# Optimization experiments

Hardware: AMD Instinct MI355X
Metric: run time of the kernel (lower is better)

The kernel has to match this reference:

```python
import jax, jax.numpy as jnp
import numpy as np

NUM_REL = 3


def _inter_layer(h_tail_all, self_tail, self_full, adj, idx, alpha):
    """One InterAgg layer (vectorized over 3 relations' IntraAgg + softmax fusion).
    h_tail_all: [N, d]  last-d features of previous layer for ALL nodes
    self_tail:  [n, d]  same features for the batch nodes
    self_full:  [n, D]  full previous-layer features for the batch nodes
    adj:        [3, N, K] neighbor indices
    idx:        [n]      batch node indices
    alpha:      [2d, 3]  relation attention params
    returns [n, D + 2d]
    """
    W = jax.nn.softmax(alpha, axis=1)  # [2d, 3]
    weighted = jnp.zeros((idx.shape[0], alpha.shape[0]), dtype=h_tail_all.dtype)
    for r in range(NUM_REL):  # fixed small structural loop
        neigh = adj[r][idx]                       # [n, K]
        mean = h_tail_all[neigh].mean(axis=1)     # [n, d]  neighbor-mean (IntraAgg _feats_1)
        intra = jnp.concatenate([mean, self_tail - mean], axis=1)  # [n, 2d]
        weighted = weighted + intra * W[:, r]     # softmax-weighted relation fusion
    return jnp.concatenate([self_full, weighted], axis=1)


def setup_inputs() -> dict:
    key = jax.random.key(0)
    ks = jax.random.split(key, 8)
    N, K, d, B = 50000, 32, 64, 1024
    return {
        "feat_data": jax.random.normal(ks[0], (N, 25), dtype=jnp.float32),
        "W_mlp": jax.random.normal(ks[1], (25, d), dtype=jnp.float32) * 0.2,
        "alpha1": jax.random.normal(ks[2], (2 * d, 3), dtype=jnp.float32) * 0.1,
        "alpha2": jax.random.normal(ks[3], (4 * d, 3), dtype=jnp.float32) * 0.1,
        "linear_w": jax.random.normal(ks[4], (7 * d, 2), dtype=jnp.float32) * 0.05,
        "prior": jax.random.uniform(ks[5], (2,), dtype=jnp.float32, minval=0.01, maxval=1.0),
        "adj": jax.random.randint(ks[6], (3, N, K), 0, N, dtype=jnp.int32),
        "nodes": jax.random.randint(ks[7], (B,), 0, N, dtype=jnp.int32),
    }


def reference(feat_data, W_mlp, alpha1, alpha2, linear_w, prior, adj, nodes):
    N = feat_data.shape[0]
    d = W_mlp.shape[1]
    # MLP layer (layer 0): per-node linear projection
    h0 = feat_data @ W_mlp                                   # [N, d]
    # InterAgg layer 1 over all nodes (so layer 2 can gather neighbor features)
    all_idx = jnp.arange(N)
    h1 = _inter_layer(h0, h0, h0, adj, all_idx, alpha1)      # [N, 3d]
    # InterAgg layer 2 over the batch nodes; uses last 2d cols of layer-1 output
    self_full = h1[nodes]                                    # [B, 3d]
    self_tail = self_full[:, -2 * d:]                        # [B, 2d]
    h2 = _inter_layer(h1[:, -2 * d:], self_tail, self_full, adj, nodes, alpha2)  # [B, 7d]
    # Final linear + log-prior
    return h2 @ linear_w + jnp.log(prior)                    # [B, 2]
```

## Files before the change

### kernel.cpp

```cpp
#include <hip/hip_runtime.h>

typedef unsigned int u32;
typedef unsigned short u16;

__device__ __forceinline__ float bf16_lo(u32 u) { u32 x = u << 16; return __builtin_bit_cast(float, x); }
__device__ __forceinline__ float bf16_hi(u32 u) { u32 x = u & 0xffff0000u; return __builtin_bit_cast(float, x); }
__device__ __forceinline__ float bf16f(u16 v) { u32 x = ((u32)v) << 16; return __builtin_bit_cast(float, x); }
__device__ __forceinline__ u16 f2bf(float f) {
    u32 x = __builtin_bit_cast(u32, f);
    return (u16)((x + 0x7fffu + ((x >> 16) & 1u)) >> 16);
}

__global__ __launch_bounds__(256) void k_prep(const float* __restrict__ feat,
                                              u16* __restrict__ featp, int N) {
    int t = blockIdx.x * 256 + threadIdx.x;
    int row = t >> 5, col = t & 31;
    if (row >= N) return;
    featp[(size_t)row * 32 + col] = (col < 25) ? f2bf(feat[(size_t)row * 25 + col]) : (u16)0;
}

__global__ __launch_bounds__(256) void k_layer1(const float* __restrict__ feat,
                                                const u16* __restrict__ featp,
                                                const float* __restrict__ Wmlp,
                                                const float* __restrict__ alpha1,
                                                const int* __restrict__ adj,
                                                u16* __restrict__ w1h, int N) {
    int wave = threadIdx.x >> 6;
    int lane = threadIdx.x & 63;
    int i = blockIdx.x * 4 + wave;
    if (i >= N) return;
    int g = lane >> 4;
    int c = lane & 15;

    float wcol[25];
#pragma unroll
    for (int k = 0; k < 25; ++k) wcol[k] = Wmlp[k * 64 + lane];

    const u32* fp = (const u32*)featp;

    float a0[3], a1[3];
#pragma unroll
    for (int r = 0; r < 3; ++r) {
        const int* arow = adj + ((size_t)r * N + i) * 32;
        float s0 = 0.f, s1 = 0.f;
#pragma unroll
        for (int it = 0; it < 8; ++it) {
            int nb = arow[it * 4 + g];
            u32 u = fp[nb * 16 + c];
            s0 += bf16_lo(u);
            s1 += bf16_hi(u);
        }
        s0 += __shfl_xor(s0, 16, 64); s0 += __shfl_xor(s0, 32, 64);
        s1 += __shfl_xor(s1, 16, 64); s1 += __shfl_xor(s1, 32, 64);
        a0[r] = s0; a1[r] = s1;
    }

    float mean[3];
#pragma unroll
    for (int r = 0; r < 3; ++r) {
        float acc = 0.f;
#pragma unroll
        for (int k = 0; k < 25; ++k) {
            int src = (k & 1) ? __builtin_bit_cast(int, a1[r]) : __builtin_bit_cast(int, a0[r]);
            float mf = __builtin_bit_cast(float, __builtin_amdgcn_readlane(src, k >> 1));
            acc += mf * wcol[k];
        }
        mean[r] = acc * (1.f / 32.f);
    }

    const float* frow = feat + (size_t)i * 25;
    float self = 0.f;
#pragma unroll
    for (int k = 0; k < 25; ++k) self += frow[k] * wcol[k];

    float et[3], eb[3], st = 0.f, sb = 0.f;
#pragma unroll
    for (int r = 0; r < 3; ++r) {
        et[r] = __expf(alpha1[lane * 3 + r]);        st += et[r];
        eb[r] = __expf(alpha1[(64 + lane) * 3 + r]); sb += eb[r];
    }
    float top = 0.f, bot = 0.f;
#pragma unroll
    for (int r = 0; r < 3; ++r) { top += et[r] * mean[r]; bot += eb[r] * mean[r]; }
    top /= st;
    bot /= sb;

    w1h[(size_t)i * 128 + lane]      = f2bf(top);
    w1h[(size_t)i * 128 + 64 + lane] = f2bf(self - bot);
}

__global__ __launch_bounds__(128) void k_layer2(const float* __restrict__ feat,
                                                const float* __restrict__ Wmlp,
                                                const u16* __restrict__ w1h,
                                                const float* __restrict__ alpha2,
                                                const float* __restrict__ lw,
                                                const float* __restrict__ prior,
                                                const int* __restrict__ adj,
                                                const int* __restrict__ nodes,
                                                float* __restrict__ out, int N) {
    __shared__ int s_idx[96];
    __shared__ float s_red[4];
    int b = blockIdx.x;
    int i = nodes[b];
    int t = threadIdx.x;

    if (t < 96) {
        int r = t >> 5, k = t & 31;
        s_idx[t] = adj[((size_t)r * N + i) * 32 + k];
    }
    __syncthreads();

    float mean[3];
#pragma unroll
    for (int r = 0; r < 3; ++r) {
        float acc = 0.f;
#pragma unroll
        for (int k = 0; k < 32; ++k)
            acc += bf16f(w1h[(size_t)s_idx[r * 32 + k] * 128 + t]);
        mean[r] = acc * (1.f / 32.f);
    }

    float et[3], eb[3], st = 0.f, sb = 0.f;
#pragma unroll
    for (int r = 0; r < 3; ++r) {
        et[r] = __expf(alpha2[t * 3 + r]);         st += et[r];
        eb[r] = __expf(alpha2[(128 + t) * 3 + r]); sb += eb[r];
    }
    float t2 = 0.f, wb = 0.f;
#pragma unroll
    for (int r = 0; r < 3; ++r) { t2 += et[r] * mean[r]; wb += eb[r] * mean[r]; }
    t2 /= st;
    wb /= sb;

    float t1 = bf16f(w1h[(size_t)i * 128 + t]);
    float t3 = t1 - wb;

    float p0 = t1 * lw[(64 + t) * 2 + 0] + t2 * lw[(192 + t) * 2 + 0] + t3 * lw[(320 + t) * 2 + 0];
    float p1 = t1 * lw[(64 + t) * 2 + 1] + t2 * lw[(192 + t) * 2 + 1] + t3 * lw[(320 + t) * 2 + 1];
    if (t < 64) {
        float t0 = 0.f;
#pragma unroll
        for (int k = 0; k < 25; ++k) t0 += feat[(size_t)i * 25 + k] * Wmlp[k * 64 + t];
        p0 += t0 * lw[t * 2 + 0];
        p1 += t0 * lw[t * 2 + 1];
    }

#pragma unroll
    for (int off = 32; off > 0; off >>= 1) {
        p0 += __shfl_down(p0, off, 64);
        p1 += __shfl_down(p1, off, 64);
    }
    int wv = t >> 6, lane = t & 63;
    if (lane == 0) { s_red[wv * 2 + 0] = p0; s_red[wv * 2 + 1] = p1; }
    __syncthreads();
    if (t == 0) {
        out[b * 2 + 0] = s_red[0] + s_red[2] + __logf(prior[0]);
        out[b * 2 + 1] = s_red[1] + s_red[3] + __logf(prior[1]);
    }
}

extern "C" void kernel_launch(void* const* d_in, const int* in_sizes, int n_in,
                              void* d_out, int out_size, void* d_ws, size_t ws_size,
                              hipStream_t stream) {
    const float* feat   = (const float*)d_in[0];
    const float* Wmlp   = (const float*)d_in[1];
    const float* alpha1 = (const float*)d_in[2];
    const float* alpha2 = (const float*)d_in[3];
    const float* lw     = (const float*)d_in[4];
    const float* prior  = (const float*)d_in[5];
    const int*   adj    = (const int*)d_in[6];
    const int*   nodes  = (const int*)d_in[7];
    float* out = (float*)d_out;

    int N = in_sizes[0] / 25;
    int B = in_sizes[7];

    u16* featp = (u16*)d_ws;
    u16* w1    = featp + (size_t)N * 32;

    k_prep  <<<(N * 32 + 255) / 256, 256, 0, stream>>>(feat, featp, N);
    k_layer1<<<(N + 3) / 4,          256, 0, stream>>>(feat, featp, Wmlp, alpha1, adj, w1, N);
    k_layer2<<<B,                    128, 0, stream>>>(feat, Wmlp, w1, alpha2, lw, prior, adj, nodes, out, N);
}
```

Baseline: 61.69 us.

## Split layer-1 into a gather pass and an MFMA projection with prefolded weights

Layer 1 is split into two kernels. The first gathers the raw neighbor feature sums for each relation, plus each node's own features, into an fp16 staging buffer. The second projects that buffer with a single MFMA matmul against a weight matrix that folds in the MLP weights, the relation softmax, the 1/32 mean and the sign of the difference term. This replaces the per-lane readlane dot products and exp work in layer 1 with matrix-core work. The cost is an extra intermediate buffer written and read back per node, two more kernel launches, and fp16 rounding of the neighbor sums.

New measurement: 66.42 us. +7.7%, slower.

```diff
diff --git a/kernel.cpp b/kernel.cpp
--- a/kernel.cpp
+++ b/kernel.cpp
@@ -2,6 +2,17 @@
 
 typedef unsigned int u32;
 typedef unsigned short u16;
+typedef _Float16 f16;
+typedef __attribute__((ext_vector_type(2))) _Float16 f16x2;
+typedef __attribute__((ext_vector_type(4))) _Float16 f16x4;
+typedef __attribute__((ext_vector_type(8))) _Float16 f16x8;
+typedef __attribute__((ext_vector_type(4))) float f32x4;
+
+#if __has_builtin(__builtin_amdgcn_mfma_f32_16x16x16f16)
+#define USE_K16 1
+#else
+#define USE_K16 0
+#endif
 
 __device__ __forceinline__ float bf16_lo(u32 u) { u32 x = u << 16; return __builtin_bit_cast(float, x); }
 __device__ __forceinline__ float bf16_hi(u32 u) { u32 x = u & 0xffff0000u; return __builtin_bit_cast(float, x); }
@@ -19,12 +30,45 @@
     featp[(size_t)row * 32 + col] = (col < 25) ? f2bf(feat[(size_t)row * 25 + col]) : (u16)0;
 }
 
-__global__ __launch_bounds__(256) void k_layer1(const float* __restrict__ feat,
+__device__ float m_val(int row, int col, const float* __restrict__ W,
+                       const float* __restrict__ a1) {
+    if (row >= 84) {
+        int k = row - 84;
+        return (k < 25 && col >= 64) ? W[k * 64 + (col - 64)] : 0.f;
+    }
+    int seg = (row >= 56) ? 2 : (row >= 28) ? 1 : 0;
+    int k = row - seg * 28;
+    if (k >= 25) return 0.f;
+    int cc = (col < 64) ? col : col - 64;
+    int arow = (col < 64) ? cc : 64 + cc;
+    float e0 = __expf(a1[arow * 3 + 0]);
+    float e1 = __expf(a1[arow * 3 + 1]);
+    float e2 = __expf(a1[arow * 3 + 2]);
+    float wt = ((seg == 0) ? e0 : (seg == 1) ? e1 : e2) / (e0 + e1 + e2);
+    float v = W[k * 64 + cc] * wt * (1.f / 32.f);
+    return (col < 64) ? v : -v;
+}
+
+__global__ __launch_bounds__(256) void k_prepM(const float* __restrict__ W,
+                                               const float* __restrict__ a1,
+                                               f16* __restrict__ Bpack) {
+    int idx = blockIdx.x * 256 + threadIdx.x;
+#if USE_K16
+    int j = idx & 3, l = (idx >> 2) & 63, ks = (idx >> 8) & 7, ct = idx >> 11;
+    int row = ks * 16 + ((l >> 4) << 2) + j;
+#else
+    int j = idx & 7, l = (idx >> 3) & 63, ks = (idx >> 9) & 3, ct = idx >> 11;
+    int row = ks * 32 + ((l >> 4) << 3) + j;
+#endif
+    int col = ct * 16 + (l & 15);
+    float v = (row < 112) ? m_val(row, col, W, a1) : 0.f;
+    Bpack[idx] = (f16)v;
+}
+
+__global__ __launch_bounds__(256) void k_gather(const float* __restrict__ feat,
                                                 const u16* __restrict__ featp,
-                                                const float* __restrict__ Wmlp,
-                                                const float* __restrict__ alpha1,
                                                 const int* __restrict__ adj,
-                                                u16* __restrict__ w1h, int N) {
+                                                f16* __restrict__ xbuf, int N) {
     int wave = threadIdx.x >> 6;
     int lane = threadIdx.x & 63;
     int i = blockIdx.x * 4 + wave;
@@ -32,13 +76,8 @@
     int g = lane >> 4;
     int c = lane & 15;
 
-    float wcol[25];
-#pragma unroll
-    for (int k = 0; k < 25; ++k) wcol[k] = Wmlp[k * 64 + lane];
-
     const u32* fp = (const u32*)featp;
 
-    float a0[3], a1[3];
 #pragma unroll
     for (int r = 0; r < 3; ++r) {
         const int* arow = adj + ((size_t)r * N + i) * 32;
@@ -52,41 +91,65 @@
         }
         s0 += __shfl_xor(s0, 16, 64); s0 += __shfl_xor(s0, 32, 64);
         s1 += __shfl_xor(s1, 16, 64); s1 += __shfl_xor(s1, 32, 64);
-        a0[r] = s0; a1[r] = s1;
-    }
-
-    float mean[3];
-#pragma unroll
-    for (int r = 0; r < 3; ++r) {
-        float acc = 0.f;
-#pragma unroll
-        for (int k = 0; k < 25; ++k) {
-            int src = (k & 1) ? __builtin_bit_cast(int, a1[r]) : __builtin_bit_cast(int, a0[r]);
-            float mf = __builtin_bit_cast(float, __builtin_amdgcn_readlane(src, k >> 1));
-            acc += mf * wcol[k];
-        }
-        mean[r] = acc * (1.f / 32.f);
-    }
-
-    const float* frow = feat + (size_t)i * 25;
-    float self = 0.f;
-#pragma unroll
-    for (int k = 0; k < 25; ++k) self += frow[k] * wcol[k];
-
-    float et[3], eb[3], st = 0.f, sb = 0.f;
-#pragma unroll
-    for (int r = 0; r < 3; ++r) {
-        et[r] = __expf(alpha1[lane * 3 + r]);        st += et[r];
-        eb[r] = __expf(alpha1[(64 + lane) * 3 + r]); sb += eb[r];
-    }
-    float top = 0.f, bot = 0.f;
-#pragma unroll
-    for (int r = 0; r < 3; ++r) { top += et[r] * mean[r]; bot += eb[r] * mean[r]; }
-    top /= st;
-    bot /= sb;
-
-    w1h[(size_t)i * 128 + lane]      = f2bf(top);
-    w1h[(size_t)i * 128 + 64 + lane] = f2bf(self - bot);
+        if (g == 0 && c < 14) {
+            f16x2 o;
+            o[0] = (f16)s0;
+            o[1] = (f16)s1;
+            *(u32*)(xbuf + (size_t)i * 128 + r * 28 + 2 * c) = __builtin_bit_cast(u32, o);
+        }
+    }
+    if (lane < 28)
+        xbuf[(size_t)i * 128 + 84 + lane] = (lane < 25) ? (f16)feat[(size_t)i * 25 + lane] : (f16)0.f;
+}
+
+__global__ __launch_bounds__(256) void k_mfma(const f16* __restrict__ xbuf,
+                                              const f16* __restrict__ Bpack,
+                                              u16* __restrict__ w1, int N) {
+    int unit = blockIdx.x * 4 + (threadIdx.x >> 6);
+    if (unit * 16 >= N) return;
+    int l = threadIdx.x & 63;
+    int i0 = unit * 16;
+#if USE_K16
+    f16x4 a[8];
+    const f16* xrow = xbuf + (size_t)(i0 + (l & 15)) * 128 + ((l >> 4) << 2);
+#pragma unroll
+    for (int ks = 0; ks < 8; ++ks) a[ks] = *(const f16x4*)(xrow + ks * 16);
+#pragma unroll
+    for (int ct = 0; ct < 8; ++ct) {
+        f32x4 d = {0.f, 0.f, 0.f, 0.f};
+        const f16* bp = Bpack + ((size_t)(ct * 8) * 64 + l) * 4;
+#pragma unroll
+        for (int ks = 0; ks < 8; ++ks) {
+            f16x4 b = *(const f16x4*)(bp + ks * 256);
+            d = __builtin_amdgcn_mfma_f32_16x16x16f16(a[ks], b, d, 0, 0, 0);
+        }
+#pragma unroll
+        for (int reg = 0; reg < 4; ++reg) {
+            int node = i0 + ((l >> 4) << 2) + reg;
+            if (node < N) w1[(size_t)node * 128 + ct * 16 + (l & 15)] = f2bf(d[reg]);
+        }
+    }
+#else
+    f16x8 a[4];
+    const f16* xrow = xbuf + (size_t)(i0 + (l & 15)) * 128 + ((l >> 4) << 3);
+#pragma unroll
+    for (int ks = 0; ks < 4; ++ks) a[ks] = *(const f16x8*)(xrow + ks * 32);
+#pragma unroll
+    for (int ct = 0; ct < 8; ++ct) {
+        f32x4 d = {0.f, 0.f, 0.f, 0.f};
+        const f16* bp = Bpack + ((size_t)(ct * 4) * 64 + l) * 8;
+#pragma unroll
+        for (int ks = 0; ks < 4; ++ks) {
+            f16x8 b = *(const f16x8*)(bp + ks * 512);
+            d = __builtin_amdgcn_mfma_f32_16x16x32_f16(a[ks], b, d, 0, 0, 0);
+        }
+#pragma unroll
+        for (int reg = 0; reg < 4; ++reg) {
+            int node = i0 + ((l >> 4) << 2) + reg;
+            if (node < N) w1[(size_t)node * 128 + ct * 16 + (l & 15)] = f2bf(d[reg]);
+        }
+    }
+#endif
 }
 
 __global__ __launch_bounds__(128) void k_layer2(const float* __restrict__ feat,
@@ -175,10 +238,15 @@
     int N = in_sizes[0] / 25;
     int B = in_sizes[7];
 
-    u16* featp = (u16*)d_ws;
-    u16* w1    = featp + (size_t)N * 32;
+    char* base = (char*)d_ws;
+    u16* featp = (u16*)base;
+    u16* w1    = (u16*)base;
+    f16* xbuf  = (f16*)(base + (size_t)N * 128 * 2);
+    f16* Bpack = (f16*)(base + (size_t)N * 128 * 2 + (size_t)N * 128 * 2);
 
     k_prep  <<<(N * 32 + 255) / 256, 256, 0, stream>>>(feat, featp, N);
-    k_layer1<<<(N + 3) / 4,          256, 0, stream>>>(feat, featp, Wmlp, alpha1, adj, w1, N);
+    k_prepM <<<64,                   256, 0, stream>>>(Wmlp, alpha1, Bpack);
+    k_gather<<<(N + 3) / 4,          256, 0, stream>>>(feat, featp, adj, xbuf, N);
+    k_mfma  <<<((N + 15) / 16 + 3) / 4, 256, 0, stream>>>(xbuf, Bpack, w1, N);
     k_layer2<<<B,                    128, 0, stream>>>(feat, Wmlp, w1, alpha2, lw, prior, adj, nodes, out, N);
 }
```
